# Optimization experiments

Hardware: AMD Instinct MI355X
Metric: run time of the kernel (lower is better)

The kernel has to match this reference:

```python
import jax, jax.numpy as jnp
import numpy as np

N, F_IN, H, C, E = 50000, 256, 4, 64, 800000
HC = H * C  # n_target_nodes = 256


def setup_inputs() -> dict:
    key = jax.random.key(0)
    ks = jax.random.split(key, 16)
    s = 1.0 / np.sqrt(F_IN)
    inp = {
        "x": jax.random.normal(ks[0], (N, F_IN), jnp.float32),
        "edge_index": jax.random.randint(ks[1], (2, E), 0, N, jnp.int64),
        "edge_attr": jax.random.uniform(ks[2], (E, 1), jnp.float32),
        "Wq": jax.random.normal(ks[3], (F_IN, HC), jnp.float32) * s,
        "bq": jnp.zeros((HC,), jnp.float32),
        "Wk": jax.random.normal(ks[4], (F_IN, HC), jnp.float32) * s,
        "bk": jnp.zeros((HC,), jnp.float32),
        "Wv": jax.random.normal(ks[5], (F_IN, HC), jnp.float32) * s,
        "bv": jnp.zeros((HC,), jnp.float32),
        "We": jax.random.normal(ks[6], (1, HC), jnp.float32),
        "be": jnp.zeros((HC,), jnp.float32),
        "Wskip": jax.random.normal(ks[7], (F_IN, HC), jnp.float32) * s,
        "bskip": jnp.zeros((HC,), jnp.float32),
        "gn_weight": jnp.ones((HC,), jnp.float32),
        "gn_bias": jnp.zeros((HC,), jnp.float32),
        "gn_mean_scale": jnp.ones((HC,), jnp.float32),
    }
    return inp


def _la_forward(x, edge_index, edge_attr, Wq, bq, Wk, bk, Wv, bv, We, be,
                Wskip, bskip, gn_weight, gn_bias, gn_mean_scale):
    n = x.shape[0]
    src, dst = edge_index[0], edge_index[1]  # message src(j) -> dst(i)
    q = (x @ Wq + bq).reshape(n, H, C)
    k = (x @ Wk + bk).reshape(n, H, C)
    v = (x @ Wv + bv).reshape(n, H, C)
    e = (edge_attr @ We + be).reshape(-1, H, C)  # [E,H,C]

    k_j = k[src] + e                              # [E,H,C]
    alpha = jnp.einsum('ehc,ehc->eh', q[dst], k_j) / jnp.sqrt(jnp.float32(C))
    # edge-softmax over incoming edges of each dst node
    amax = jax.ops.segment_max(alpha, dst, num_segments=n)      # [N,H]
    ex = jnp.exp(alpha - amax[dst])
    denom = jax.ops.segment_sum(ex, dst, num_segments=n)        # [N,H]
    attn = ex / (denom[dst] + 1e-16)                            # [E,H]

    msg = (v[src] + e) * attn[:, :, None]                       # [E,H,C]
    out = jax.ops.segment_sum(msg, dst, num_segments=n).reshape(n, HC)
    out = out + x @ Wskip + bskip                               # root/skip

    # GraphNorm (single graph batch)
    mean = out.mean(axis=0)
    centered = out - gn_mean_scale * mean
    var = (centered * centered).mean(axis=0)
    out = centered / jnp.sqrt(var + 1e-5) * gn_weight + gn_bias

    out = jax.nn.relu(out)
    xt = out.T @ out                                            # [HC,HC]
    xt_min, xt_max = jnp.min(xt), jnp.max(xt)
    xt = (xt - xt_min) / (xt_max - xt_min + 1e-8)
    return xt


def reference(x, edge_index, edge_attr, Wq, bq, Wk, bk, Wv, bv, We, be,
              Wskip, bskip, gn_weight, gn_bias, gn_mean_scale):
    return _la_forward(x, edge_index, edge_attr, Wq, bq, Wk, bk, Wv, bv,
                       We, be, Wskip, bskip, gn_weight, gn_bias, gn_mean_scale)
```

## Files before the change

kernel.cpp:

```cpp
#include <hip/hip_runtime.h>
#include <math.h>


typedef float f32x4 __attribute__((ext_vector_type(4)));
typedef short s16x8 __attribute__((ext_vector_type(8)));

static __device__ __forceinline__ unsigned short f2bf(float f) {
    unsigned int u = __float_as_uint(f);
    unsigned int r = u + 0x7FFFu + ((u >> 16) & 1u);
    return (unsigned short)(r >> 16);
}
static __device__ __forceinline__ float bf2f(unsigned short u) {
    return __uint_as_float(((unsigned int)u) << 16);
}
static __device__ __forceinline__ float blo(unsigned int u) {
    return __uint_as_float(u << 16);
}
static __device__ __forceinline__ float bhi(unsigned int u) {
    return __uint_as_float(u & 0xffff0000u);
}

#define LOG2E_8 0.18033688011112042f

__global__ void la_x2bf(const float* __restrict__ x, unsigned short* __restrict__ xb,
                        int total4)
{
    int i = blockIdx.x * blockDim.x + threadIdx.x;
    int stride = gridDim.x * blockDim.x;
    for (; i < total4; i += stride) {
        float4 v = ((const float4*)x)[i];
        ushort4 o;
        o.x = f2bf(v.x); o.y = f2bf(v.y); o.z = f2bf(v.z); o.w = f2bf(v.w);
        ((ushort4*)xb)[i] = o;
    }
}

__global__ __launch_bounds__(256) void la_wprep2(
    const float* __restrict__ Wq, const float* __restrict__ Wk,
    const float* __restrict__ Wv, const float* __restrict__ Ws,
    const float* __restrict__ bq, const float* __restrict__ bk,
    const float* __restrict__ bv, const float* __restrict__ bs,
    unsigned short* __restrict__ wt, float* __restrict__ bcat)
{
    __shared__ float T[64][68];
    const int bid = blockIdx.x;
    const int m  = bid >> 4;
    const int kt = (bid >> 2) & 3, ct = bid & 3;
    const int k0 = kt * 64, c0 = ct * 64;
    const float* W = (m == 0) ? Wq : (m == 1) ? Wk : (m == 2) ? Wv : Ws;
    const float* B = (m == 0) ? bq : (m == 1) ? bk : (m == 2) ? bv : bs;
    const int t = threadIdx.x;

#pragma unroll
    for (int it = 0; it < 4; ++it) {
        int s = it * 256 + t;
        int r = s >> 4;
        int q = (s & 15) * 4;
        float4 v = *(const float4*)(W + (size_t)(k0 + r) * 256 + c0 + q);
        T[r][q + 0] = v.x; T[r][q + 1] = v.y;
        T[r][q + 2] = v.z; T[r][q + 3] = v.w;
    }
    __syncthreads();
#pragma unroll
    for (int it = 0; it < 4; ++it) {
        int s = it * 256 + t;
        int c = s >> 4;
        int kq = (s & 15) * 4;
        ushort4 o;
        o.x = f2bf(T[kq + 0][c]); o.y = f2bf(T[kq + 1][c]);
        o.z = f2bf(T[kq + 2][c]); o.w = f2bf(T[kq + 3][c]);
        *(ushort4*)(wt + (size_t)(m * 256 + c0 + c) * 256 + k0 + kq) = o;
    }
    if (kt == 0 && t < 64) bcat[m * 256 + c0 + t] = B[c0 + t];
}

__global__ __launch_bounds__(256) void la_gemm_mfma(
    const unsigned short* __restrict__ xb, const unsigned short* __restrict__ wt,
    const float* __restrict__ bcat,
    unsigned short* __restrict__ qarr, unsigned short* __restrict__ kv,
    unsigned short* __restrict__ skiparr, int n)
{
    __shared__ __align__(16) unsigned short As[128 * 40];
    __shared__ __align__(16) unsigned short Bs[128 * 40];

    const int row0 = blockIdx.x * 128;
    const int col0 = blockIdx.y * 128;
    const int msel = blockIdx.y >> 1;
    const int t = threadIdx.x;
    const int l = t & 63;
    const int w = t >> 6;
    const int wr = w >> 1, wc = w & 1;
    const int l15 = l & 15, l4 = l >> 4;

    f32x4 acc[4][4];
#pragma unroll
    for (int i = 0; i < 4; ++i)
#pragma unroll
        for (int j = 0; j < 4; ++j) acc[i][j] = (f32x4){0.f, 0.f, 0.f, 0.f};

    for (int k0 = 0; k0 < 256; k0 += 32) {
#pragma unroll
        for (int c2 = 0; c2 < 2; ++c2) {
            int chunk = t + c2 * 256;
            int r  = chunk >> 2;
            int ko = (chunk & 3) * 8;
            int ga = row0 + r;
            s16x8 va = (s16x8){0,0,0,0,0,0,0,0};
            if (ga < n) va = *(const s16x8*)(xb + (size_t)ga * 256 + k0 + ko);
            *(s16x8*)(As + r * 40 + ko) = va;
            int gb = col0 + r;
            s16x8 vb = *(const s16x8*)(wt + (size_t)gb * 256 + k0 + ko);
            *(s16x8*)(Bs + r * 40 + ko) = vb;
        }
        __syncthreads();
        s16x8 af[4], bfr[4];
#pragma unroll
        for (int f = 0; f < 4; ++f) {
            af[f]  = *(const s16x8*)(As + (wr * 64 + f * 16 + l15) * 40 + l4 * 8);
            bfr[f] = *(const s16x8*)(Bs + (wc * 64 + f * 16 + l15) * 40 + l4 * 8);
        }
#pragma unroll
        for (int fm = 0; fm < 4; ++fm)
#pragma unroll
            for (int fn = 0; fn < 4; ++fn)
                acc[fm][fn] = __builtin_amdgcn_mfma_f32_16x16x32_bf16(
                    af[fm], bfr[fn], acc[fm][fn], 0, 0, 0);
        __syncthreads();
    }

#pragma unroll
    for (int fm = 0; fm < 4; ++fm) {
#pragma unroll
        for (int fn = 0; fn < 4; ++fn) {
            int gc = col0 + wc * 64 + fn * 16 + l15;
            int c  = gc & 255;
            float bb = bcat[gc];
#pragma unroll
            for (int j = 0; j < 4; ++j) {
                int gr = row0 + wr * 64 + fm * 16 + l4 * 4 + j;
                if (gr >= n) continue;
                unsigned short val = f2bf(acc[fm][fn][j] + bb);
                if (msel == 0) {
                    qarr[(size_t)gr * 256 + c] = val;
                } else if (msel == 3) {
                    skiparr[(size_t)gr * 256 + c] = val;
                } else {
                    int hh = c >> 6, ch = c & 63;
                    size_t idx = (size_t)gr * 512 + hh * 128 + (ch >> 2) * 8
                               + (ch & 3) + ((msel == 2) ? 4 : 0);
                    kv[idx] = val;
                }
            }
        }
    }
}

__global__ void la_hist(const int* __restrict__ dst, int e, int* __restrict__ deg)
{
    int i = blockIdx.x * blockDim.x + threadIdx.x;
    int stride = gridDim.x * blockDim.x;
    for (; i < e; i += stride) atomicAdd(&deg[dst[i]], 1);
}

__global__ void la_chunksum(const int* __restrict__ deg, int n, int* __restrict__ part)
{
    int b = blockIdx.x, t = threadIdx.x;
    int i = b * 256 + t;
    int v = (i < n) ? deg[i] : 0;
#pragma unroll
    for (int mask = 32; mask >= 1; mask >>= 1) v += __shfl_xor(v, mask);
    __shared__ int ws[4];
    if ((t & 63) == 0) ws[t >> 6] = v;
    __syncthreads();
    if (t == 0) part[b] = ws[0] + ws[1] + ws[2] + ws[3];
}

__global__ void la_scanpart(int* __restrict__ part, int nb)
{
    __shared__ int s[256];
    int t = threadIdx.x;
    int v = (t < nb) ? part[t] : 0;
    int orig = v;
    s[t] = v;
    __syncthreads();
    for (int o = 1; o < 256; o <<= 1) {
        int u = (t >= o) ? s[t - o] : 0;
        __syncthreads();
        s[t] += u;
        __syncthreads();
    }
    if (t < nb) part[t] = s[t] - orig;
}

__global__ void la_scanfinal(const int* __restrict__ deg, int n,
                             const int* __restrict__ part, int* __restrict__ offs,
                             int* __restrict__ cursor, int e)
{
    int b = blockIdx.x, t = threadIdx.x;
    int i = b * 256 + t;
    int d = (i < n) ? deg[i] : 0;
    int v = d;
#pragma unroll
    for (int o = 1; o < 64; o <<= 1) {
        int u = __shfl_up(v, o);
        if ((t & 63) >= o) v += u;
    }
    __shared__ int wt[4];
    if ((t & 63) == 63) wt[t >> 6] = v;
    __syncthreads();
    int add = 0;
    for (int wv = 0; wv < (t >> 6); ++wv) add += wt[wv];
    int excl = v + add - d + part[b];
    if (i < n) { offs[i] = excl; cursor[i] = excl; }
    if (b == 0 && t == 0) offs[n] = e;
}

__global__ void la_scatter(const int* __restrict__ src, const int* __restrict__ dst,
                           const float* __restrict__ ea, int e,
                           int* __restrict__ cursor, uint2* __restrict__ rec)
{
    int i = blockIdx.x * blockDim.x + threadIdx.x;
    int stride = gridDim.x * blockDim.x;
    for (; i < e; i += stride) {
        int d = dst[i];
        int pos = atomicAdd(&cursor[d], 1);
        rec[pos] = make_uint2((unsigned int)src[i], __float_as_uint(ea[i]));
    }
}

__global__ __launch_bounds__(256) void la_attn3(
    const unsigned short* __restrict__ qarr,
    const unsigned short* __restrict__ kv,
    const unsigned short* __restrict__ skiparr,
    const uint2* __restrict__ rec,
    const int* __restrict__ offs,
    const float* __restrict__ We, const float* __restrict__ be,
    unsigned short* __restrict__ outb)
{
    const int node = blockIdx.x;
    const int t = threadIdx.x;
    const int h = t >> 6;
    const int l = t & 63;
    const int quarter = l >> 4;
    const int lc = l & 15;
    const int cb = h * 64 + lc * 4;

    uint2 qp = *(const uint2*)(qarr + (size_t)node * 256 + cb);
    const float q0 = blo(qp.x), q1 = bhi(qp.x);
    const float q2 = blo(qp.y), q3 = bhi(qp.y);
    float4 we4 = *(const float4*)(We + cb);
    float4 be4 = *(const float4*)(be + cb);

    float pw = fmaf(q3, we4.w, fmaf(q2, we4.z, fmaf(q1, we4.y, q0 * we4.x)));
    float pb = fmaf(q3, be4.w, fmaf(q2, be4.z, fmaf(q1, be4.y, q0 * be4.x)));
#pragma unroll
    for (int mask = 1; mask <= 8; mask <<= 1) {
        pw += __shfl_xor(pw, mask);
        pb += __shfl_xor(pb, mask);
    }
    const float qWe8 = pw * LOG2E_8;
    const float qbe8 = pb * LOG2E_8;

    const int start = offs[node], end = offs[node + 1];
    const int koff = h * 128 + lc * 8;

    float lsum = 0.f, Sfa = 0.f;
    float a0 = 0.f, a1 = 0.f, a2 = 0.f, a3 = 0.f;

    for (int j0 = start; j0 < end; j0 += 4) {
        int j = j0 + quarter;
        bool valid = (j < end);
        int jj = valid ? j : j0;
        uint2 r = rec[jj];
        int   s   = (int)r.x;
        float eaj = __uint_as_float(r.y);
        uint4 kvu = *(const uint4*)(kv + (((size_t)s) << 9) + koff);
        float k0 = blo(kvu.x), k1 = bhi(kvu.x);
        float k2 = blo(kvu.y), k3 = bhi(kvu.y);
        float d = fmaf(q3, k3, fmaf(q2, k2, fmaf(q1, k1, q0 * k0)));
#pragma unroll
        for (int mask = 1; mask <= 8; mask <<= 1) d += __shfl_xor(d, mask);
        float aL = fmaf(d, LOG2E_8, fmaf(eaj, qWe8, qbe8));
        aL = valid ? aL : -INFINITY;
        float f = exp2f(aL);
        lsum += f;
        Sfa = fmaf(f, eaj, Sfa);
        float v0 = blo(kvu.z), v1 = bhi(kvu.z);
        float v2 = blo(kvu.w), v3 = bhi(kvu.w);
        a0 = fmaf(f, v0, a0);
        a1 = fmaf(f, v1, a1);
        a2 = fmaf(f, v2, a2);
        a3 = fmaf(f, v3, a3);
    }

#pragma unroll
    for (int mask = 16; mask <= 32; mask <<= 1) {
        lsum += __shfl_xor(lsum, mask);
        Sfa  += __shfl_xor(Sfa,  mask);
        a0   += __shfl_xor(a0,   mask);
        a1   += __shfl_xor(a1,   mask);
        a2   += __shfl_xor(a2,   mask);
        a3   += __shfl_xor(a3,   mask);
    }

    if (quarter == 0) {
        float inv = 1.f / (lsum + 1e-16f);
        uint2 sp = *(const uint2*)(skiparr + (size_t)node * 256 + cb);
        ushort4 o;
        o.x = f2bf(fmaf(we4.x, Sfa, fmaf(be4.x, lsum, a0)) * inv + blo(sp.x));
        o.y = f2bf(fmaf(we4.y, Sfa, fmaf(be4.y, lsum, a1)) * inv + bhi(sp.x));
        o.z = f2bf(fmaf(we4.z, Sfa, fmaf(be4.z, lsum, a2)) * inv + blo(sp.y));
        o.w = f2bf(fmaf(we4.w, Sfa, fmaf(be4.w, lsum, a3)) * inv + bhi(sp.y));
        *(ushort4*)(outb + (size_t)node * 256 + cb) = o;
    }
}

__global__ __launch_bounds__(256) void la_colsum(
    const unsigned short* __restrict__ outb, float* __restrict__ cs,
    float* __restrict__ cs2, int n)
{
    const int col = threadIdx.x;
    const int r0 = blockIdx.x * 64;
    const int rend = (r0 + 64 < n) ? r0 + 64 : n;
    float s = 0.f, s2 = 0.f;
    for (int r = r0; r < rend; ++r) {
        float vv = bf2f(outb[(size_t)r * 256 + col]);
        s += vv;
        s2 = fmaf(vv, vv, s2);
    }
    atomicAdd(&cs[col], s);
    atomicAdd(&cs2[col], s2);
}

__global__ __launch_bounds__(256) void la_gram_mfma(
    const unsigned short* __restrict__ outb,
    const float* __restrict__ cs, const float* __restrict__ cs2,
    const float* __restrict__ gnw, const float* __restrict__ gnb,
    const float* __restrict__ gms,
    float* __restrict__ xt, int n, int kchunk)
{
    __shared__ __align__(16) unsigned int Ta[128 * 20];
    __shared__ __align__(16) unsigned int Tb[128 * 20];

    const int bx = blockIdx.x;
    const int kc   = bx / 3;
    const int tile = bx - kc * 3;
    const int i0 = (tile == 2) ? 128 : 0;
    const int j0 = (tile == 0) ? 0 : 128;
    const bool diag = (tile != 1);
    const int kbeg = kc * kchunk;
    if (kbeg >= n) return;
    const int kend = (kbeg + kchunk < n) ? kbeg + kchunk : n;

    const int t = threadIdx.x;
    const int l = t & 63, w = t >> 6;
    const int wr = w >> 1, wc = w & 1;
    const int l15 = l & 15, l4 = l >> 4;

    const int kp  = t >> 4;
    const int cg8 = t & 15;

    const float invn = 1.f / (float)n;
    float Ai[8], Bi[8], Aj[8], Bj[8];
#pragma unroll
    for (int j = 0; j < 8; ++j) {
        {
            int ci = i0 + cg8 * 8 + j;
            float mean = cs[ci] * invn;
            float m2   = cs2[ci] * invn;
            float s    = gms[ci];
            float var  = m2 - 2.f * s * mean * mean + s * s * mean * mean;
            float a    = gnw[ci] / sqrtf(var + 1e-5f);
            Ai[j] = a; Bi[j] = gnb[ci] - s * mean * a;
        }
        {
            int cj = j0 + cg8 * 8 + j;
            float mean = cs[cj] * invn;
            float m2   = cs2[cj] * invn;
            float s    = gms[cj];
            float var  = m2 - 2.f * s * mean * mean + s * s * mean * mean;
            float a    = gnw[cj] / sqrtf(var + 1e-5f);
            Aj[j] = a; Bj[j] = gnb[cj] - s * mean * a;
        }
    }

    f32x4 acc[4][4];
#pragma unroll
    for (int i = 0; i < 4; ++i)
#pragma unroll
        for (int j = 0; j < 4; ++j) acc[i][j] = (f32x4){0.f, 0.f, 0.f, 0.f};

    const int nsteps = (kend - kbeg + 31) >> 5;
    for (int ks = 0; ks < nsteps; ++ks) {
        const int gr0 = kbeg + ks * 32 + kp * 2;
        const bool v0 = (gr0 < kend), v1 = (gr0 + 1 < kend);

        {
            uint4 u0 = make_uint4(0,0,0,0), u1 = make_uint4(0,0,0,0);
            if (v0) u0 = *(const uint4*)(outb + (size_t)gr0 * 256 + i0 + cg8 * 8);
            if (v1) u1 = *(const uint4*)(outb + (size_t)(gr0+1) * 256 + i0 + cg8 * 8);
            float xs[8] = {blo(u0.x),bhi(u0.x),blo(u0.y),bhi(u0.y),
                           blo(u0.z),bhi(u0.z),blo(u0.w),bhi(u0.w)};
            float ys[8] = {blo(u1.x),bhi(u1.x),blo(u1.y),bhi(u1.y),
                           blo(u1.z),bhi(u1.z),blo(u1.w),bhi(u1.w)};
#pragma unroll
            for (int j = 0; j < 8; ++j) {
                float r0 = v0 ? fmaxf(fmaf(xs[j], Ai[j], Bi[j]), 0.f) : 0.f;
                float r1 = v1 ? fmaxf(fmaf(ys[j], Ai[j], Bi[j]), 0.f) : 0.f;
                int c = cg8 * 8 + j;
                unsigned int u = (unsigned int)f2bf(r0)
                               | ((unsigned int)f2bf(r1) << 16);
                Ta[c * 20 + (kp ^ (((c >> 3) & 3) << 2))] = u;
            }
        }
        if (!diag) {
            uint4 u0 = make_uint4(0,0,0,0), u1 = make_uint4(0,0,0,0);
            if (v0) u0 = *(const uint4*)(outb + (size_t)gr0 * 256 + j0 + cg8 * 8);
            if (v1) u1 = *(const uint4*)(outb + (size_t)(gr0+1) * 256 + j0 + cg8 * 8);
            float xs[8] = {blo(u0.x),bhi(u0.x),blo(u0.y),bhi(u0.y),
                           blo(u0.z),bhi(u0.z),blo(u0.w),bhi(u0.w)};
            float ys[8] = {blo(u1.x),bhi(u1.x),blo(u1.y),bhi(u1.y),
                           blo(u1.z),bhi(u1.z),blo(u1.w),bhi(u1.w)};
#pragma unroll
            for (int j = 0; j < 8; ++j) {
                float r0 = v0 ? fmaxf(fmaf(xs[j], Aj[j], Bj[j]), 0.f) : 0.f;
                float r1 = v1 ? fmaxf(fmaf(ys[j], Aj[j], Bj[j]), 0.f) : 0.f;
                int c = cg8 * 8 + j;
                unsigned int u = (unsigned int)f2bf(r0)
                               | ((unsigned int)f2bf(r1) << 16);
                Tb[c * 20 + (kp ^ (((c >> 3) & 3) << 2))] = u;
            }
        }
        __syncthreads();

        const unsigned int* TB = diag ? Ta : Tb;
        s16x8 af[4], bfr[4];
#pragma unroll
        for (int f = 0; f < 4; ++f) {
            int ca = wr * 64 + f * 16 + l15;
            af[f] = *(const s16x8*)(Ta + ca * 20 + ((l4 * 4) ^ (((ca >> 3) & 3) << 2)));
            int cb2 = wc * 64 + f * 16 + l15;
            bfr[f] = *(const s16x8*)(TB + cb2 * 20 + ((l4 * 4) ^ (((cb2 >> 3) & 3) << 2)));
        }
#pragma unroll
        for (int fm = 0; fm < 4; ++fm)
#pragma unroll
            for (int fn = 0; fn < 4; ++fn)
                acc[fm][fn] = __builtin_amdgcn_mfma_f32_16x16x32_bf16(
                    af[fm], bfr[fn], acc[fm][fn], 0, 0, 0);
        __syncthreads();
    }

#pragma unroll
    for (int fm = 0; fm < 4; ++fm)
#pragma unroll
        for (int fn = 0; fn < 4; ++fn) {
            int col = j0 + wc * 64 + fn * 16 + l15;
#pragma unroll
            for (int j = 0; j < 4; ++j) {
                int row = i0 + wr * 64 + fm * 16 + l4 * 4 + j;
                float vv = acc[fm][fn][j];
                atomicAdd(&xt[(size_t)row * 256 + col], vv);
                if (tile == 1)
                    atomicAdd(&xt[(size_t)col * 256 + row], vv);
            }
        }
}

__global__ __launch_bounds__(256) void la_minmax_part(
    const float* __restrict__ xt, float* __restrict__ mmp)
{
    const int b = blockIdx.x, t = threadIdx.x;
    float mn = INFINITY, mx = -INFINITY;
#pragma unroll
    for (int k = 0; k < 2; ++k) {
        float4 v = ((const float4*)xt)[b * 512 + k * 256 + t];
        mn = fminf(mn, fminf(fminf(v.x, v.y), fminf(v.z, v.w)));
        mx = fmaxf(mx, fmaxf(fmaxf(v.x, v.y), fmaxf(v.z, v.w)));
    }
#pragma unroll
    for (int mask = 32; mask >= 1; mask >>= 1) {
        mn = fminf(mn, __shfl_xor(mn, mask));
        mx = fmaxf(mx, __shfl_xor(mx, mask));
    }
    __shared__ float smn[4], smx[4];
    if ((t & 63) == 0) { smn[t >> 6] = mn; smx[t >> 6] = mx; }
    __syncthreads();
    if (t == 0) {
        mn = fminf(fminf(smn[0], smn[1]), fminf(smn[2], smn[3]));
        mx = fmaxf(fmaxf(smx[0], smx[1]), fmaxf(smx[2], smx[3]));
        mmp[b * 2]     = mn;
        mmp[b * 2 + 1] = mx;
    }
}

__global__ void la_norm(float* __restrict__ xt, const float* __restrict__ mmp)
{
    float mn = INFINITY, mx = -INFINITY;
#pragma unroll
    for (int i = 0; i < 32; ++i) {
        mn = fminf(mn, mmp[i * 2]);
        mx = fmaxf(mx, mmp[i * 2 + 1]);
    }
    float inv = 1.f / (mx - mn + 1e-8f);
    int i = blockIdx.x * blockDim.x + threadIdx.x;
    xt[i] = (xt[i] - mn) * inv;
}

extern "C" void kernel_launch(void* const* d_in, const int* in_sizes, int n_in,
                              void* d_out, int out_size, void* d_ws, size_t ws_size,
                              hipStream_t stream)
{
    const float* x   = (const float*)d_in[0];
    const int*   ei  = (const int*)  d_in[1];
    const float* ea  = (const float*)d_in[2];
    const float* Wq  = (const float*)d_in[3];
    const float* bq  = (const float*)d_in[4];
    const float* Wk  = (const float*)d_in[5];
    const float* bk  = (const float*)d_in[6];
    const float* Wv  = (const float*)d_in[7];
    const float* bv  = (const float*)d_in[8];
    const float* We  = (const float*)d_in[9];
    const float* be  = (const float*)d_in[10];
    const float* Ws  = (const float*)d_in[11];
    const float* bs  = (const float*)d_in[12];
    const float* gnw = (const float*)d_in[13];
    const float* gnb = (const float*)d_in[14];
    const float* gms = (const float*)d_in[15];

    const int n = in_sizes[0] / 256;
    const int e = in_sizes[1] / 2;
    const int* srcI = ei;
    const int* dstI = ei + e;

    char* ws = (char*)d_ws;
    size_t off = 0;
    auto take = [&](size_t bytes) -> void* {
        void* p = (void*)(ws + off);
        off += (bytes + 255) & ~(size_t)255;
        return p;
    };
    unsigned short* xb    = (unsigned short*)take((size_t)n * 256 * 2);
    unsigned short* wtbuf = (unsigned short*)take((size_t)1024 * 256 * 2);
    float*          bcat  = (float*)take(1024 * 4);
    unsigned short* qarr  = (unsigned short*)take((size_t)n * 256 * 2);
    unsigned short* kv    = (unsigned short*)take((size_t)n * 512 * 2);
    unsigned short* skipb = (unsigned short*)take((size_t)n * 256 * 2);
    unsigned short* outb  = (unsigned short*)take((size_t)n * 256 * 2);
    int*   deg    = (int*)  take((size_t)n * 4);
    int*   cursor = (int*)  take((size_t)n * 4);
    int*   offs   = (int*)  take((size_t)(n + 1) * 4);
    int*   part   = (int*)  take(256 * 4);
    uint2* csrR   = (uint2*)take((size_t)e * 8);
    float* cs     = (float*)take(256 * 4);
    float* cs2    = (float*)take(256 * 4);
    float* mmp    = (float*)take(64 * 4);
    (void)ws_size; (void)n_in; (void)out_size;

    float* xt = (float*)d_out;

    hipMemsetAsync(deg, 0, (size_t)n * 4, stream);
    hipMemsetAsync(cs,  0, 256 * 4, stream);
    hipMemsetAsync(cs2, 0, 256 * 4, stream);
    hipMemsetAsync(xt,  0, (size_t)65536 * 4, stream);

    la_x2bf  <<<2048, 256, 0, stream>>>(x, xb, n * 64);
    la_wprep2<<<64, 256, 0, stream>>>(Wq, Wk, Wv, Ws, bq, bk, bv, bs, wtbuf, bcat);

    dim3 gg((n + 127) / 128, 8);
    la_gemm_mfma<<<gg, 256, 0, stream>>>(xb, wtbuf, bcat, qarr, kv, skipb, n);

    const int nchunk = (n + 255) / 256;
    la_hist     <<<1024, 256, 0, stream>>>(dstI, e, deg);
    la_chunksum <<<nchunk, 256, 0, stream>>>(deg, n, part);
    la_scanpart <<<1, 256, 0, stream>>>(part, nchunk);
    la_scanfinal<<<nchunk, 256, 0, stream>>>(deg, n, part, offs, cursor, e);
    la_scatter  <<<1024, 256, 0, stream>>>(srcI, dstI, ea, e, cursor, csrR);

    la_attn3<<<n, 256, 0, stream>>>(qarr, kv, skipb, csrR, offs, We, be, outb);

    la_colsum<<<(n + 63) / 64, 256, 0, stream>>>(outb, cs, cs2, n);

    const int KSPLIT = 64;
    int kchunk = ((n + KSPLIT - 1) / KSPLIT + 31) & ~31;
    la_gram_mfma<<<3 * KSPLIT, 256, 0, stream>>>(outb, cs, cs2, gnw, gnb, gms,
                                                 xt, n, kchunk);

    la_minmax_part<<<32, 256, 0, stream>>>(xt, mmp);
    la_norm<<<256, 256, 0, stream>>>(xt, mmp);
}
```

Measured before the change: 460.5 us.

## Fuse prep kernels with histogram and scatter edges via recorded atomic positions

Merges the x-to-bf16 conversion, the weight transpose and the degree histogram into one heterogeneous launch. The histogram now records each edge's slot from its atomic, so the scatter needs no second round of atomics or cursor array. It also zeroes deg, cs and cs2 with a single memset and doubles the K-split of the Gram kernel. The cost is an extra E-sized pos buffer to write and read, plus more partial atomic adds into xt from the larger split.

```diff
diff --git a/kernel.cpp b/kernel.cpp
--- a/kernel.cpp
+++ b/kernel.cpp
@@ -22,56 +22,63 @@
 
 #define LOG2E_8 0.18033688011112042f
 
-__global__ void la_x2bf(const float* __restrict__ x, unsigned short* __restrict__ xb,
-                        int total4)
-{
-    int i = blockIdx.x * blockDim.x + threadIdx.x;
-    int stride = gridDim.x * blockDim.x;
-    for (; i < total4; i += stride) {
-        float4 v = ((const float4*)x)[i];
-        ushort4 o;
-        o.x = f2bf(v.x); o.y = f2bf(v.y); o.z = f2bf(v.z); o.w = f2bf(v.w);
-        ((ushort4*)xb)[i] = o;
-    }
-}
-
-__global__ __launch_bounds__(256) void la_wprep2(
+__global__ __launch_bounds__(256) void la_prep(
+    const float* __restrict__ x, int total4,
     const float* __restrict__ Wq, const float* __restrict__ Wk,
     const float* __restrict__ Wv, const float* __restrict__ Ws,
     const float* __restrict__ bq, const float* __restrict__ bk,
     const float* __restrict__ bv, const float* __restrict__ bs,
-    unsigned short* __restrict__ wt, float* __restrict__ bcat)
+    unsigned short* __restrict__ wt, float* __restrict__ bcat,
+    const int* __restrict__ dst, int e,
+    int* __restrict__ deg, int* __restrict__ pos,
+    unsigned short* __restrict__ xb)
 {
     __shared__ float T[64][68];
     const int bid = blockIdx.x;
-    const int m  = bid >> 4;
-    const int kt = (bid >> 2) & 3, ct = bid & 3;
-    const int k0 = kt * 64, c0 = ct * 64;
-    const float* W = (m == 0) ? Wq : (m == 1) ? Wk : (m == 2) ? Wv : Ws;
-    const float* B = (m == 0) ? bq : (m == 1) ? bk : (m == 2) ? bv : bs;
     const int t = threadIdx.x;
 
-#pragma unroll
-    for (int it = 0; it < 4; ++it) {
-        int s = it * 256 + t;
-        int r = s >> 4;
-        int q = (s & 15) * 4;
-        float4 v = *(const float4*)(W + (size_t)(k0 + r) * 256 + c0 + q);
-        T[r][q + 0] = v.x; T[r][q + 1] = v.y;
-        T[r][q + 2] = v.z; T[r][q + 3] = v.w;
-    }
-    __syncthreads();
-#pragma unroll
-    for (int it = 0; it < 4; ++it) {
-        int s = it * 256 + t;
-        int c = s >> 4;
-        int kq = (s & 15) * 4;
-        ushort4 o;
-        o.x = f2bf(T[kq + 0][c]); o.y = f2bf(T[kq + 1][c]);
-        o.z = f2bf(T[kq + 2][c]); o.w = f2bf(T[kq + 3][c]);
-        *(ushort4*)(wt + (size_t)(m * 256 + c0 + c) * 256 + k0 + kq) = o;
-    }
-    if (kt == 0 && t < 64) bcat[m * 256 + c0 + t] = B[c0 + t];
+    if (bid < 64) {
+        const int m  = bid >> 4;
+        const int kt = (bid >> 2) & 3, ct = bid & 3;
+        const int k0 = kt * 64, c0 = ct * 64;
+        const float* W = (m == 0) ? Wq : (m == 1) ? Wk : (m == 2) ? Wv : Ws;
+        const float* B = (m == 0) ? bq : (m == 1) ? bk : (m == 2) ? bv : bs;
+#pragma unroll
+        for (int it = 0; it < 4; ++it) {
+            int s = it * 256 + t;
+            int r = s >> 4;
+            int q = (s & 15) * 4;
+            float4 v = *(const float4*)(W + (size_t)(k0 + r) * 256 + c0 + q);
+            T[r][q + 0] = v.x; T[r][q + 1] = v.y;
+            T[r][q + 2] = v.z; T[r][q + 3] = v.w;
+        }
+        __syncthreads();
+#pragma unroll
+        for (int it = 0; it < 4; ++it) {
+            int s = it * 256 + t;
+            int c = s >> 4;
+            int kq = (s & 15) * 4;
+            ushort4 o;
+            o.x = f2bf(T[kq + 0][c]); o.y = f2bf(T[kq + 1][c]);
+            o.z = f2bf(T[kq + 2][c]); o.w = f2bf(T[kq + 3][c]);
+            *(ushort4*)(wt + (size_t)(m * 256 + c0 + c) * 256 + k0 + kq) = o;
+        }
+        if (kt == 0 && t < 64) bcat[m * 256 + c0 + t] = B[c0 + t];
+    } else if (bid < 1088) {
+        int i = (bid - 64) * 256 + t;
+        const int stride = 1024 * 256;
+        for (; i < e; i += stride)
+            pos[i] = atomicAdd(&deg[dst[i]], 1);
+    } else {
+        int i = (bid - 1088) * 256 + t;
+        const int stride = 2048 * 256;
+        for (; i < total4; i += stride) {
+            float4 v = ((const float4*)x)[i];
+            ushort4 o;
+            o.x = f2bf(v.x); o.y = f2bf(v.y); o.z = f2bf(v.z); o.w = f2bf(v.w);
+            ((ushort4*)xb)[i] = o;
+        }
+    }
 }
 
 __global__ __launch_bounds__(256) void la_gemm_mfma(
@@ -155,13 +162,6 @@
     }
 }
 
-__global__ void la_hist(const int* __restrict__ dst, int e, int* __restrict__ deg)
-{
-    int i = blockIdx.x * blockDim.x + threadIdx.x;
-    int stride = gridDim.x * blockDim.x;
-    for (; i < e; i += stride) atomicAdd(&deg[dst[i]], 1);
-}
-
 __global__ void la_chunksum(const int* __restrict__ deg, int n, int* __restrict__ part)
 {
     int b = blockIdx.x, t = threadIdx.x;
@@ -194,7 +194,7 @@
 
 __global__ void la_scanfinal(const int* __restrict__ deg, int n,
                              const int* __restrict__ part, int* __restrict__ offs,
-                             int* __restrict__ cursor, int e)
+                             int e)
 {
     int b = blockIdx.x, t = threadIdx.x;
     int i = b * 256 + t;
@@ -211,20 +211,22 @@
     int add = 0;
     for (int wv = 0; wv < (t >> 6); ++wv) add += wt[wv];
     int excl = v + add - d + part[b];
-    if (i < n) { offs[i] = excl; cursor[i] = excl; }
+    if (i < n) offs[i] = excl;
     if (b == 0 && t == 0) offs[n] = e;
 }
 
-__global__ void la_scatter(const int* __restrict__ src, const int* __restrict__ dst,
-                           const float* __restrict__ ea, int e,
-                           int* __restrict__ cursor, uint2* __restrict__ rec)
+__global__ void la_scatter2(const int* __restrict__ src, const int* __restrict__ dst,
+                            const float* __restrict__ ea,
+                            const int* __restrict__ pos,
+                            const int* __restrict__ offs, int e,
+                            uint2* __restrict__ rec)
 {
     int i = blockIdx.x * blockDim.x + threadIdx.x;
     int stride = gridDim.x * blockDim.x;
     for (; i < e; i += stride) {
         int d = dst[i];
-        int pos = atomicAdd(&cursor[d], 1);
-        rec[pos] = make_uint2((unsigned int)src[i], __float_as_uint(ea[i]));
+        int p = offs[d] + pos[i];
+        rec[p] = make_uint2((unsigned int)src[i], __float_as_uint(ea[i]));
     }
 }
 
@@ -540,6 +542,11 @@
         off += (bytes + 255) & ~(size_t)255;
         return p;
     };
+    int*   deg    = (int*)  take((size_t)n * 4);
+    float* cs     = (float*)take(256 * 4);
+    float* cs2    = (float*)take(256 * 4);
+    size_t zero_bytes = off;
+
     unsigned short* xb    = (unsigned short*)take((size_t)n * 256 * 2);
     unsigned short* wtbuf = (unsigned short*)take((size_t)1024 * 256 * 2);
     float*          bcat  = (float*)take(1024 * 4);
@@ -547,41 +554,36 @@
     unsigned short* kv    = (unsigned short*)take((size_t)n * 512 * 2);
     unsigned short* skipb = (unsigned short*)take((size_t)n * 256 * 2);
     unsigned short* outb  = (unsigned short*)take((size_t)n * 256 * 2);
-    int*   deg    = (int*)  take((size_t)n * 4);
-    int*   cursor = (int*)  take((size_t)n * 4);
+    int*   pos    = (int*)  take((size_t)e * 4);
     int*   offs   = (int*)  take((size_t)(n + 1) * 4);
     int*   part   = (int*)  take(256 * 4);
     uint2* csrR   = (uint2*)take((size_t)e * 8);
-    float* cs     = (float*)take(256 * 4);
-    float* cs2    = (float*)take(256 * 4);
     float* mmp    = (float*)take(64 * 4);
     (void)ws_size; (void)n_in; (void)out_size;
 
     float* xt = (float*)d_out;
 
-    hipMemsetAsync(deg, 0, (size_t)n * 4, stream);
-    hipMemsetAsync(cs,  0, 256 * 4, stream);
-    hipMemsetAsync(cs2, 0, 256 * 4, stream);
+    hipMemsetAsync(deg, 0, zero_bytes, stream);
     hipMemsetAsync(xt,  0, (size_t)65536 * 4, stream);
 
-    la_x2bf  <<<2048, 256, 0, stream>>>(x, xb, n * 64);
-    la_wprep2<<<64, 256, 0, stream>>>(Wq, Wk, Wv, Ws, bq, bk, bv, bs, wtbuf, bcat);
+    la_prep<<<3136, 256, 0, stream>>>(x, n * 64,
+                                      Wq, Wk, Wv, Ws, bq, bk, bv, bs,
+                                      wtbuf, bcat, dstI, e, deg, pos, xb);
 
     dim3 gg((n + 127) / 128, 8);
     la_gemm_mfma<<<gg, 256, 0, stream>>>(xb, wtbuf, bcat, qarr, kv, skipb, n);
 
     const int nchunk = (n + 255) / 256;
-    la_hist     <<<1024, 256, 0, stream>>>(dstI, e, deg);
     la_chunksum <<<nchunk, 256, 0, stream>>>(deg, n, part);
     la_scanpart <<<1, 256, 0, stream>>>(part, nchunk);
-    la_scanfinal<<<nchunk, 256, 0, stream>>>(deg, n, part, offs, cursor, e);
-    la_scatter  <<<1024, 256, 0, stream>>>(srcI, dstI, ea, e, cursor, csrR);
+    la_scanfinal<<<nchunk, 256, 0, stream>>>(deg, n, part, offs, e);
+    la_scatter2 <<<1024, 256, 0, stream>>>(srcI, dstI, ea, pos, offs, e, csrR);
 
     la_attn3<<<n, 256, 0, stream>>>(qarr, kv, skipb, csrR, offs, We, be, outb);
 
     la_colsum<<<(n + 63) / 64, 256, 0, stream>>>(outb, cs, cs2, n);
 
-    const int KSPLIT = 64;
+    const int KSPLIT = 128;
     int kchunk = ((n + KSPLIT - 1) / KSPLIT + 31) & ~31;
     la_gram_mfma<<<3 * KSPLIT, 256, 0, stream>>>(outb, cs, cs2, gnw, gnb, gms,
                                                  xt, n, kchunk);
```

Result: faster. 410.8 us (-10.8%).
